# Kernel tuning notes

Measured on AMD Instinct MI355X. Metric: run time of the kernel, lower is better.

The kernel has to match this reference:

```python
import jax, jax.numpy as jnp
import numpy as np

B, T, C, H, W = 1, 8, 64, 96, 96
DG = 16  # deform groups
MAX_RES = 5.0  # max_residue_magnitude


def lrelu(x):
    return jnp.where(x >= 0, x, 0.1 * x)


def conv(x, w, b):
    y = jax.lax.conv_general_dilated(x, w, (1, 1), 'SAME',
                                     dimension_numbers=('NCHW', 'OIHW', 'NCHW'))
    return y + b[None, :, None, None]


def mod_deform_conv2d(x, offset, mask, weight, bias, dg):
    # Modulated deformable conv v2: 3x3 kernel, stride 1, pad 1, dil 1.
    Bs, Cin, Hs, Ws = x.shape
    K = 9
    cpg = Cin // dg
    Cout = weight.shape[0]
    off = offset.reshape(Bs, dg, K, 2, Hs, Ws)  # (y, x) per tap
    m = mask.reshape(Bs, dg, K, Hs, Ws)
    ky = jnp.repeat(jnp.arange(3), 3).astype(x.dtype)
    kx = jnp.tile(jnp.arange(3), 3).astype(x.dtype)
    # base sampling positions: out_pos - pad + tap*dil
    py = (jnp.arange(Hs, dtype=x.dtype) - 1.0)[None, :, None] + ky[:, None, None]  # (K,H,1)
    px = (jnp.arange(Ws, dtype=x.dtype) - 1.0)[None, None, :] + kx[:, None, None]  # (K,1,W)
    sy = off[:, :, :, 0] + py  # (B,dg,K,H,W)
    sx = off[:, :, :, 1] + px
    y0 = jnp.floor(sy)
    x0 = jnp.floor(sx)
    fy = sy - y0
    fx = sx - x0
    y0i = y0.astype(jnp.int32)
    x0i = x0.astype(jnp.int32)
    xf = x.reshape(Bs, dg, cpg, Hs * Ws)

    def gather(yi, xi, wgt):
        valid = (yi >= 0) & (yi < Hs) & (xi >= 0) & (xi < Ws)
        idx = (jnp.clip(yi, 0, Hs - 1) * Ws + jnp.clip(xi, 0, Ws - 1))
        idx = idx.reshape(Bs, dg, 1, K * Hs * Ws)
        v = jnp.take_along_axis(xf, idx, axis=3).reshape(Bs, dg, cpg, K, Hs, Ws)
        return v * (wgt * valid)[:, :, None]

    val = (gather(y0i, x0i, (1 - fy) * (1 - fx))
           + gather(y0i, x0i + 1, (1 - fy) * fx)
           + gather(y0i + 1, x0i, fy * (1 - fx))
           + gather(y0i + 1, x0i + 1, fy * fx))
    cols = val * m[:, :, None]  # (B,dg,cpg,K,H,W)
    wr = weight.reshape(Cout, dg, cpg, K)
    out = jnp.einsum('ogck,bgckhw->bohw', wr, cols)
    return out + bias[None, :, None, None]


def deform_align(xin, cond, p):
    h = lrelu(conv(cond, p['ow1'], p['ob1']))
    h = lrelu(conv(h, p['ow2'], p['ob2']))
    h = lrelu(conv(h, p['ow3'], p['ob3']))
    out = conv(h, p['ow4'], p['ob4'])
    offset = MAX_RES * jnp.tanh(out[:, :18 * DG])
    mask = jax.nn.sigmoid(out[:, 18 * DG:])
    return mod_deform_conv2d(xin, offset, mask, p['dw'], p['db'], DG)


def bidir_prop(x, params):
    t = x.shape[1]
    spatial = [x[:, i] for i in range(t)]
    feats = {}
    for name, rev in (('backward_', True), ('forward_', False)):
        p = params[name]
        order = list(range(t))[::-1] if rev else list(range(t))
        out_list = []
        prop = jnp.zeros_like(spatial[0])
        for i, idx in enumerate(order):
            cur = spatial[idx]
            if i > 0:
                feat_n2 = out_list[-2] if i > 1 else jnp.zeros_like(prop)
                cond = jnp.concatenate([prop, cur, feat_n2], axis=1)
                prop = deform_align(jnp.concatenate([prop, feat_n2], axis=1), cond, p)
            if name == 'forward_':
                feat = jnp.concatenate([cur, feats['backward_'][idx], prop], axis=1)
            else:
                feat = jnp.concatenate([cur, prop], axis=1)
            prop = prop + conv(lrelu(conv(feat, p['bw1'], p['bb1'])), p['bw2'], p['bb2'])
            out_list.append(prop)
        feats[name] = out_list[::-1] if rev else out_list
    fw, fb = params['fusion']
    outs = [conv(jnp.concatenate([feats['backward_'][i], feats['forward_'][i]], axis=1), fw, fb)
            for i in range(t)]
    return jnp.stack(outs, axis=1) + x


def setup_inputs() -> dict:
    key = jax.random.key(0)
    ks = iter(jax.random.split(key, 64))

    def w(*shape):
        return jax.random.normal(next(ks), shape, jnp.float32) * 0.03

    def b(n):
        return jnp.zeros((n,), jnp.float32)

    d = {'x': jax.random.normal(next(ks), (B, T, C, H, W), jnp.float32)}
    for pre, bb1_in in (('b', 2 * C), ('f', 3 * C)):
        d[pre + '_dw'] = w(C, 2 * C, 3, 3); d[pre + '_db'] = b(C)
        d[pre + '_ow1'] = w(C, 3 * C, 3, 3); d[pre + '_ob1'] = b(C)
        d[pre + '_ow2'] = w(C, C, 3, 3); d[pre + '_ob2'] = b(C)
        d[pre + '_ow3'] = w(C, C, 3, 3); d[pre + '_ob3'] = b(C)
        d[pre + '_ow4'] = w(27 * DG, C, 3, 3); d[pre + '_ob4'] = b(27 * DG)
        d[pre + '_bw1'] = w(C, bb1_in, 3, 3); d[pre + '_bb1'] = b(C)
        d[pre + '_bw2'] = w(C, C, 3, 3); d[pre + '_bb2'] = b(C)
    d['fus_w'] = w(C, 2 * C, 1, 1)
    d['fus_b'] = b(C)
    return d


def _assemble(b_dw, b_db, b_ow1, b_ob1, b_ow2, b_ob2, b_ow3, b_ob3, b_ow4, b_ob4,
              b_bw1, b_bb1, b_bw2, b_bb2,
              f_dw, f_db, f_ow1, f_ob1, f_ow2, f_ob2, f_ow3, f_ob3, f_ow4, f_ob4,
              f_bw1, f_bb1, f_bw2, f_bb2, fus_w, fus_b):
    return {
        'backward_': dict(dw=b_dw, db=b_db, ow1=b_ow1, ob1=b_ob1, ow2=b_ow2, ob2=b_ob2,
                          ow3=b_ow3, ob3=b_ob3, ow4=b_ow4, ob4=b_ob4,
                          bw1=b_bw1, bb1=b_bb1, bw2=b_bw2, bb2=b_bb2),
        'forward_': dict(dw=f_dw, db=f_db, ow1=f_ow1, ob1=f_ob1, ow2=f_ow2, ob2=f_ob2,
                         ow3=f_ow3, ob3=f_ob3, ow4=f_ow4, ob4=f_ob4,
                         bw1=f_bw1, bb1=f_bb1, bw2=f_bw2, bb2=f_bb2),
        'fusion': (fus_w, fus_b),
    }


def reference(x, b_dw, b_db, b_ow1, b_ob1, b_ow2, b_ob2, b_ow3, b_ob3, b_ow4, b_ob4,
              b_bw1, b_bb1, b_bw2, b_bb2,
              f_dw, f_db, f_ow1, f_ob1, f_ow2, f_ob2, f_ow3, f_ob3, f_ow4, f_ob4,
              f_bw1, f_bb1, f_bw2, f_bb2, fus_w, fus_b):
    params = _assemble(b_dw, b_db, b_ow1, b_ob1, b_ow2, b_ob2, b_ow3, b_ob3, b_ow4, b_ob4,
                       b_bw1, b_bb1, b_bw2, b_bb2,
                       f_dw, f_db, f_ow1, f_ob1, f_ow2, f_ob2, f_ow3, f_ob3, f_ow4, f_ob4,
                       f_bw1, f_bb1, f_bw2, f_bb2, fus_w, fus_b)
    return bidir_prop(x, params)
```

## Files before the change

### kernel.cpp

```cpp
#include <hip/hip_runtime.h>
#include <cstddef>
#include <cstdint>

#define HW96 9216
#define FRAME (64 * 9216)

typedef unsigned short ushort_t;
typedef __attribute__((ext_vector_type(8))) short bf16x8;
typedef __attribute__((ext_vector_type(4))) float f32x4;
typedef __attribute__((ext_vector_type(4))) unsigned u32x4;
typedef __attribute__((ext_vector_type(8))) ushort_t u16x8;
typedef __attribute__((ext_vector_type(4))) ushort_t u16x4;

__device__ __forceinline__ float unpk(unsigned p) {
    return __uint_as_float(p & 0xFFFF0000u) + __uint_as_float(p << 16);
}
__device__ __forceinline__ unsigned pk(float v) {
    unsigned u = __float_as_uint(v);
    unsigned hi = u & 0xFFFF0000u;
    float rem = v - __uint_as_float(hi);
    unsigned r = __float_as_uint(rem);
    unsigned lo = (r + 0x7FFFu + ((r >> 16) & 1u)) >> 16;
    return hi | (lo & 0xFFFFu);
}
__device__ __forceinline__ void split16(float v, ushort_t& h, ushort_t& l) {
    unsigned u = __float_as_uint(v);
    h = (ushort_t)(u >> 16);
    float rem = v - __uint_as_float(u & 0xFFFF0000u);
    unsigned r = __float_as_uint(rem);
    l = (ushort_t)((r + 0x7FFFu + ((r >> 16) & 1u)) >> 16);
}
__device__ __forceinline__ ushort_t bf16rnd(float v) {
    unsigned u = __float_as_uint(v);
    return (ushort_t)((u + 0x7FFFu + ((u >> 16) & 1u)) >> 16);
}
__device__ __forceinline__ float bfh(ushort_t h) {
    return __uint_as_float(((unsigned)h) << 16);
}

struct FragJob { const float* src; ushort_t* dst; int O, I, OT, KC, mode; };
struct FragJobs { FragJob j[15]; };

__global__ __launch_bounds__(256) void frag_all_k(FragJobs jobs) {
    const FragJob& J = jobs.j[blockIdx.y];
    int idx = blockIdx.x * 256 + threadIdx.x;
    int total = ((J.mode == 0) ? 9 : 1) * J.KC * J.OT * 512;
    if (idx >= total) return;
    int jj = idx & 7;
    int lane = (idx >> 3) & 63;
    int rem = idx >> 9;
    int ot = rem % J.OT;
    rem /= J.OT;
    int cc = rem % J.KC;
    int t = rem / J.KC;
    int o = ot * 16 + (lane & 15);
    float wv = 0.f;
    if (J.mode == 0) {
        int ci = cc * 32 + (lane >> 4) * 8 + jj;
        if (o < J.O && ci < J.I) wv = J.src[(o * J.I + ci) * 9 + t];
    } else if (J.mode == 1) {
        int K = cc * 32 + (lane >> 4) * 8 + jj;
        int g = K / 72, r2 = K % 72;
        int tap = r2 >> 3, c = r2 & 7;
        int ci = g * 8 + c;
        if (o < J.O && ci < J.I) wv = J.src[(o * J.I + ci) * 9 + tap];
    } else {
        int ci = cc * 32 + (lane >> 4) * 8 + jj;
        if (o < J.O && ci < J.I) wv = J.src[o * J.I + ci];
    }
    ushort_t h, l;
    split16(wv, h, l);
    J.dst[idx] = h;
    J.dst[total + idx] = l;
}

__global__ __launch_bounds__(256) void pack_tr_k(const float* __restrict__ src,
                                                 unsigned* __restrict__ dst,
                                                 ushort_t* __restrict__ dsth) {
    const int t = blockIdx.y;
    const int px0 = blockIdx.x * 64;
    __shared__ unsigned tile[64 * 65];
    const float* s = src + (size_t)t * FRAME;
    unsigned* d = dst + (size_t)t * FRAME;
    ushort_t* dh = dsth + (size_t)t * FRAME;
#pragma unroll
    for (int it = 0; it < 16; ++it) {
        int e = it * 256 + threadIdx.x;
        int p = e & 63, ch = e >> 6;
        tile[ch * 65 + p] = pk(s[(size_t)ch * HW96 + px0 + p]);
    }
    __syncthreads();
#pragma unroll
    for (int it = 0; it < 16; ++it) {
        int e = it * 256 + threadIdx.x;
        int ch = e & 63, p = e >> 6;
        unsigned v = tile[ch * 65 + p];
        d[(size_t)(px0 + p) * 64 + ch] = v;
        dh[(size_t)(px0 + p) * 64 + ch] = (ushort_t)(v >> 16);
    }
}

template <int TERMS>
__global__ __launch_bounds__(128, 3) void convm_k(
    const unsigned* __restrict__ s0, const unsigned* __restrict__ s1,
    int nsrc, int dslot, const float* __restrict__ dpacc,
    const float* __restrict__ ddbias, const ushort_t* __restrict__ wfrag,
    int KCfull, const float* __restrict__ bias,
    const float* __restrict__ addsrc, const float* __restrict__ addsrc2,
    const float* __restrict__ abias, ushort_t* __restrict__ outhi,
    unsigned* __restrict__ outpk, int act) {
    const int tid = threadIdx.x;
    const int lane = tid & 63;
    const int w = tid >> 6;
    const int h = blockIdx.x & 1;
    const int bseg = blockIdx.x >> 1;
    const int ot = h * 2 + w;
    const int xb = (bseg % 6) * 16;
    const int y = bseg / 6;
    const int n = lane & 15;
    const int quad = lane >> 4;

    __shared__ __align__(16) ushort_t ldsH[3 * 18 * 72];
    __shared__ __align__(16) ushort_t ldsL[3 * 18 * 72];

    int jst[4], jok[4], joff[4], jbase[4];
#pragma unroll
    for (int i = 0; i < 4; ++i) {
        int e = tid + i * 128;
        int rc = e >> 3, cg = e & 7;
        int r = rc / 18, col = rc - r * 18;
        int gy = y - 1 + r, gx = xb - 1 + col;
        jst[i] = (e < 432);
        jok[i] = jst[i] && ((unsigned)gy < 96u) && ((unsigned)gx < 96u);
        joff[i] = (gy * 96 + gx) * 64 + cg * 8;
        jbase[i] = rc * 72 + cg * 8;
    }

    f32x4 acc0, acc1;
#pragma unroll
    for (int r = 0; r < 4; ++r) { acc0[r] = 0.f; acc1[r] = 0.f; }

    const size_t hlOff = (size_t)9 * KCfull * 4 * 512;

    for (int j = 0; j < nsrc; ++j) {
        const int base = j * 2;
        __syncthreads();
        if (j == dslot) {
#pragma unroll
            for (int i = 0; i < 4; ++i) {
                if (jst[i]) {
                    ushort_t hh[8], ll[8];
                    if (jok[i]) {
                        const int cg8 = ((tid + i * 128) & 7) << 3;
                        f32x4 a0 = *(const f32x4*)(dpacc + joff[i]);
                        f32x4 a1 = *(const f32x4*)(dpacc + joff[i] + 4);
                        f32x4 b0 = *(const f32x4*)(dpacc + FRAME + joff[i]);
                        f32x4 b1 = *(const f32x4*)(dpacc + FRAME + joff[i] + 4);
                        f32x4 d0 = *(const f32x4*)(ddbias + cg8);
                        f32x4 d1 = *(const f32x4*)(ddbias + cg8 + 4);
#pragma unroll
                        for (int q = 0; q < 4; ++q) {
                            split16(a0[q] + b0[q] + d0[q], hh[q], ll[q]);
                            split16(a1[q] + b1[q] + d1[q], hh[4 + q], ll[4 + q]);
                        }
                    } else {
#pragma unroll
                        for (int q = 0; q < 8; ++q) { hh[q] = 0; ll[q] = 0; }
                    }
                    u32x4 H, L;
#pragma unroll
                    for (int q = 0; q < 4; ++q) {
                        H[q] = (unsigned)hh[2 * q] | ((unsigned)hh[2 * q + 1] << 16);
                        L[q] = (unsigned)ll[2 * q] | ((unsigned)ll[2 * q + 1] << 16);
                    }
                    *(u32x4*)(ldsH + jbase[i]) = H;
                    *(u32x4*)(ldsL + jbase[i]) = L;
                }
            }
        } else {
            const unsigned* sv = (j == 0) ? s0 : s1;
#pragma unroll
            for (int i = 0; i < 4; ++i) {
                if (jst[i]) {
                    u32x4 a, b;
                    if (jok[i]) {
                        a = *(const u32x4*)(sv + joff[i]);
                        b = *(const u32x4*)(sv + joff[i] + 4);
                    } else {
#pragma unroll
                        for (int q = 0; q < 4; ++q) { a[q] = 0; b[q] = 0; }
                    }
                    u32x4 H, L;
#pragma unroll
                    for (int q = 0; q < 2; ++q) {
                        H[q] = (a[2 * q] >> 16) | (a[2 * q + 1] & 0xFFFF0000u);
                        L[q] = (a[2 * q] & 0xFFFFu) | (a[2 * q + 1] << 16);
                        H[2 + q] = (b[2 * q] >> 16) | (b[2 * q + 1] & 0xFFFF0000u);
                        L[2 + q] = (b[2 * q] & 0xFFFFu) | (b[2 * q + 1] << 16);
                    }
                    *(u32x4*)(ldsH + jbase[i]) = H;
                    *(u32x4*)(ldsL + jbase[i]) = L;
                }
            }
        }
        __syncthreads();
        bf16x8 pAh[5], pAl[5], pBh[5], pBl[5];
#pragma unroll
        for (int s = 0; s < 23; ++s) {
            if (s >= 5) {
                const int u = s - 5;
                const bf16x8 Ah = pAh[u % 5];
                const bf16x8 Bh = pBh[u % 5], Bl = pBl[u % 5];
                if (u & 1) {
                    acc1 = __builtin_amdgcn_mfma_f32_16x16x32_bf16(Ah, Bh, acc1, 0, 0, 0);
                    if (TERMS == 3)
                        acc1 = __builtin_amdgcn_mfma_f32_16x16x32_bf16(pAl[u % 5], Bh, acc1, 0, 0, 0);
                    acc1 = __builtin_amdgcn_mfma_f32_16x16x32_bf16(Ah, Bl, acc1, 0, 0, 0);
                } else {
                    acc0 = __builtin_amdgcn_mfma_f32_16x16x32_bf16(Ah, Bh, acc0, 0, 0, 0);
                    if (TERMS == 3)
                        acc0 = __builtin_amdgcn_mfma_f32_16x16x32_bf16(pAl[u % 5], Bh, acc0, 0, 0, 0);
                    acc0 = __builtin_amdgcn_mfma_f32_16x16x32_bf16(Ah, Bl, acc0, 0, 0, 0);
                }
            }
            if (s < 18) {
                const int t = s >> 1, cc2 = s & 1;
                const int ky = t / 3, kx = t % 3;
                const int ccor = base + cc2;
                const ushort_t* ab =
                    wfrag + (((size_t)(t * KCfull + ccor) * 4 + ot) * 64 + lane) * 8;
                pAh[s % 5] = *(const bf16x8*)ab;
                if (TERMS == 3) pAl[s % 5] = *(const bf16x8*)(ab + hlOff);
                const int lb = (ky * 18 + n + kx) * 72 + cc2 * 32 + quad * 8;
                pBh[s % 5] = *(const bf16x8*)(ldsH + lb);
                pBl[s % 5] = *(const bf16x8*)(ldsL + lb);
            }
        }
    }

    const int px = y * 96 + xb + n;
    f32x4 pa, pb;
#pragma unroll
    for (int r = 0; r < 4; ++r) { pa[r] = 0.f; pb[r] = 0.f; }
    if (addsrc) {
        pa = *(const f32x4*)(addsrc + (size_t)px * 64 + ot * 16 + quad * 4);
        pb = *(const f32x4*)(addsrc2 + (size_t)px * 64 + ot * 16 + quad * 4);
    }
    u16x4 hi4;
#pragma unroll
    for (int r = 0; r < 4; ++r) {
        int cout = ot * 16 + quad * 4 + r;
        float v = acc0[r] + acc1[r] + bias[cout];
        if (act) v = (v >= 0.f) ? v : 0.1f * v;
        if (addsrc) v += pa[r] + pb[r] + abias[cout];
        outpk[(size_t)px * 64 + cout] = pk(v);
        hi4[r] = bf16rnd(v);
    }
    if (outhi)
        *(u16x4*)(outhi + (size_t)px * 64 + ot * 16 + quad * 4) = hi4;
}

__global__ __launch_bounds__(128, 3) void convh_k(
    const ushort_t* __restrict__ s0, const ushort_t* __restrict__ s1,
    const ushort_t* __restrict__ s2, int b0, int b1, int b2, int nsrc,
    const ushort_t* __restrict__ wfrag, int KCfull,
    const float* __restrict__ bias, ushort_t* __restrict__ outhi, int act) {
    const int tid = threadIdx.x;
    const int lane = tid & 63;
    const int w = tid >> 6;
    const int h = blockIdx.x & 1;
    const int bseg = blockIdx.x >> 1;
    const int ot = h * 2 + w;
    const int xb = (bseg % 6) * 16;
    const int y = bseg / 6;
    const int n = lane & 15;
    const int quad = lane >> 4;

    __shared__ __align__(16) ushort_t ldsH[3 * 18 * 72];

    int jst[4], jok[4], joff[4], jbase[4];
#pragma unroll
    for (int i = 0; i < 4; ++i) {
        int e = tid + i * 128;
        int rc = e >> 3, cg = e & 7;
        int r = rc / 18, col = rc - r * 18;
        int gy = y - 1 + r, gx = xb - 1 + col;
        jst[i] = (e < 432);
        jok[i] = jst[i] && ((unsigned)gy < 96u) && ((unsigned)gx < 96u);
        joff[i] = (gy * 96 + gx) * 64 + cg * 8;
        jbase[i] = rc * 72 + cg * 8;
    }

    f32x4 acc0, acc1;
#pragma unroll
    for (int r = 0; r < 4; ++r) { acc0[r] = 0.f; acc1[r] = 0.f; }

    for (int j = 0; j < nsrc; ++j) {
        const ushort_t* sv = (j == 0) ? s0 : (j == 1 ? s1 : s2);
        const int base = (j == 0) ? b0 : (j == 1 ? b1 : b2);
        __syncthreads();
#pragma unroll
        for (int i = 0; i < 4; ++i) {
            if (jst[i]) {
                u16x8 a;
                if (jok[i]) {
                    a = *(const u16x8*)(sv + joff[i]);
                } else {
#pragma unroll
                    for (int q = 0; q < 8; ++q) a[q] = 0;
                }
                *(u16x8*)(ldsH + jbase[i]) = a;
            }
        }
        __syncthreads();
        bf16x8 pAh[5], pBh[5];
#pragma unroll
        for (int s = 0; s < 23; ++s) {
            if (s >= 5) {
                const int u = s - 5;
                const bf16x8 Ah = pAh[u % 5];
                const bf16x8 Bh = pBh[u % 5];
                if (u & 1)
                    acc1 = __builtin_amdgcn_mfma_f32_16x16x32_bf16(Ah, Bh, acc1, 0, 0, 0);
                else
                    acc0 = __builtin_amdgcn_mfma_f32_16x16x32_bf16(Ah, Bh, acc0, 0, 0, 0);
            }
            if (s < 18) {
                const int t = s >> 1, cc2 = s & 1;
                const int ky = t / 3, kx = t % 3;
                const int ccor = base + cc2;
                const ushort_t* ab =
                    wfrag + (((size_t)(t * KCfull + ccor) * 4 + ot) * 64 + lane) * 8;
                pAh[s % 5] = *(const bf16x8*)ab;
                const int lb = (ky * 18 + n + kx) * 72 + cc2 * 32 + quad * 8;
                pBh[s % 5] = *(const bf16x8*)(ldsH + lb);
            }
        }
    }

    const int px = y * 96 + xb + n;
    u16x4 hi4;
#pragma unroll
    for (int r = 0; r < 4; ++r) {
        int cout = ot * 16 + quad * 4 + r;
        float v = acc0[r] + acc1[r] + bias[cout];
        if (act) v = (v >= 0.f) ? v : 0.1f * v;
        hi4[r] = bf16rnd(v);
    }
    *(u16x4*)(outhi + (size_t)px * 64 + ot * 16 + quad * 4) = hi4;
}

__global__ __launch_bounds__(256) void dconv_fused_k(
    const ushort_t* __restrict__ sAh, const ushort_t* __restrict__ sBh,
    const ushort_t* __restrict__ hAh, const ushort_t* __restrict__ w4,
    const float* __restrict__ ob4, const ushort_t* __restrict__ dwf,
    int ngr4, float* __restrict__ pacc) {
    const int tid = threadIdx.x;
    const int lane = tid & 63;
    const int w = tid >> 6;
    const int h = blockIdx.x & 1;
    const int seg = blockIdx.x >> 1;
    const int xb = (seg % 6) * 16;
    const int y = seg / 6;
    const int n = lane & 15;
    const int quad = lane >> 4;

    __shared__ __align__(16) char smem[15232 + 9472];
    float* rawS = (float*)smem;
    ushort_t* ldsAH = (ushort_t*)(smem + 15232);
    ushort_t* colsH = (ushort_t*)(smem + 15232);

    const int nrounds = ngr4 >> 1;
    const int ng = nrounds * 4;
    const int g0 = h * ng;
    const int otO_s = (g0 * 18) >> 4;
    const int otO_e = (g0 * 18 + ng * 18 - 1) >> 4;
    const int nO = otO_e - otO_s + 1;
    const int otM_s = (288 + g0 * 9) >> 4;
    const int otM_e = (288 + g0 * 9 + ng * 9 - 1) >> 4;
    const int nM = otM_e - otM_s + 1;
    const int nt = nO + nM;
    const int rowOffO = otO_s * 16;
    const int rowOffM = otM_s * 16 - nO * 16;

#pragma unroll
    for (int i = 0; i < 2; ++i) {
        int e = tid + i * 256;
        if (e < 432) {
            int rc = e >> 3, cg = e & 7;
            int r = rc / 18, col = rc - r * 18;
            int gy = y - 1 + r, gx = xb - 1 + col;
            bool ok = ((unsigned)gy < 96u) && ((unsigned)gx < 96u);
            u16x8 a;
            if (ok) {
                a = *(const u16x8*)(hAh + (gy * 96 + gx) * 64 + cg * 8);
            } else {
#pragma unroll
                for (int q = 0; q < 8; ++q) a[q] = 0;
            }
            *(u16x8*)(ldsAH + rc * 72 + cg * 8) = a;
        }
    }
    __syncthreads();

#pragma unroll 1
    for (int j = 0; j < 4; ++j) {
        const int idx = j * 4 + w;
        if (idx >= nt) break;
        const int ot = (idx < nO) ? (otO_s + idx) : (otM_s + (idx - nO));
        f32x4 a0, a1;
#pragma unroll
        for (int r = 0; r < 4; ++r) { a0[r] = 0.f; a1[r] = 0.f; }
        bf16x8 pAh[5], pBh[5];
#pragma unroll
        for (int s = 0; s < 23; ++s) {
            if (s >= 5) {
                const int u = s - 5;
                const bf16x8 Ah = pAh[u % 5];
                const bf16x8 Bh = pBh[u % 5];
                if (u & 1)
                    a1 = __builtin_amdgcn_mfma_f32_16x16x32_bf16(Ah, Bh, a1, 0, 0, 0);
                else
                    a0 = __builtin_amdgcn_mfma_f32_16x16x32_bf16(Ah, Bh, a0, 0, 0, 0);
            }
            if (s < 18) {
                const int t = s >> 1, cc2 = s & 1;
                const int ky = t / 3, kx = t % 3;
                const ushort_t* ab =
                    w4 + (((size_t)s * 28 + ot) * 64 + lane) * 8;
                pAh[s % 5] = *(const bf16x8*)ab;
                const int lb = (ky * 18 + n + kx) * 72 + cc2 * 32 + quad * 8;
                pBh[s % 5] = *(const bf16x8*)(ldsAH + lb);
            }
        }
#pragma unroll
        for (int r = 0; r < 4; ++r) {
            int cout = ot * 16 + quad * 4 + r;
            float v = a0[r] + a1[r] + (cout < 432 ? ob4[cout] : 0.f);
            rawS[(idx * 16 + quad * 4 + r) * 17 + n] = v;
        }
    }

    f32x4 acc0, acc1;
#pragma unroll
    for (int r = 0; r < 4; ++r) { acc0[r] = 0.f; acc1[r] = 0.f; }

    for (int gci = 0; gci < nrounds; ++gci) {
        const int gc = h * nrounds + gci;
        __syncthreads();
#pragma unroll
        for (int i = 0; i < 3; ++i) {
            int e = tid + i * 256;
            if (e < 576) {
                int p = e & 15;
                int r = e >> 4;
                int gl = r / 9, k = r - gl * 9;
                int g = gc * 4 + gl;
                float ry = rawS[(g * 18 + k * 2 + 0 - rowOffO) * 17 + p];
                float rx = rawS[(g * 18 + k * 2 + 1 - rowOffO) * 17 + p];
                float rm = rawS[(288 + g * 9 + k - rowOffM) * 17 + p];
                float oy = 5.f * (1.f - 2.f / (1.f + __expf(2.f * ry)));
                float ox = 5.f * (1.f - 2.f / (1.f + __expf(2.f * rx)));
                float m = 1.f / (1.f + __expf(-rm));
                float sy = oy + (float)(y - 1 + k / 3);
                float sx = ox + (float)(xb + p - 1 + k % 3);
                float fy0 = floorf(sy), fx0 = floorf(sx);
                float fy = sy - fy0, fx = sx - fx0;
                int y0 = (int)fy0, x0 = (int)fx0;
                int y1 = y0 + 1, x1 = x0 + 1;
                bool vy0 = (unsigned)y0 < 96u, vy1 = (unsigned)y1 < 96u;
                bool vx0 = (unsigned)x0 < 96u, vx1 = (unsigned)x1 < 96u;
                int cy0 = min(max(y0, 0), 95), cy1 = min(max(y1, 0), 95);
                int cx0 = min(max(x0, 0), 95), cx1 = min(max(x1, 0), 95);
                float w00 = (1.f - fy) * (1.f - fx) * ((vy0 && vx0) ? 1.f : 0.f);
                float w01 = (1.f - fy) * fx * ((vy0 && vx1) ? 1.f : 0.f);
                float w10 = fy * (1.f - fx) * ((vy1 && vx0) ? 1.f : 0.f);
                float w11 = fy * fx * ((vy1 && vx1) ? 1.f : 0.f);
                const ushort_t* src = (g < 8) ? sAh : sBh;
                int cb = (g & 7) * 8;
                int kbase = p * 296 + gl * 72 + k * 8;
                ushort_t hh[8];
                if (src) {
                    u16x8 c00 = *(const u16x8*)(src + (cy0 * 96 + cx0) * 64 + cb);
                    u16x8 c01 = *(const u16x8*)(src + (cy0 * 96 + cx1) * 64 + cb);
                    u16x8 c10 = *(const u16x8*)(src + (cy1 * 96 + cx0) * 64 + cb);
                    u16x8 c11 = *(const u16x8*)(src + (cy1 * 96 + cx1) * 64 + cb);
#pragma unroll
                    for (int c = 0; c < 8; ++c) {
                        float v = w00 * bfh(c00[c]) + w01 * bfh(c01[c]) +
                                  w10 * bfh(c10[c]) + w11 * bfh(c11[c]);
                        hh[c] = bf16rnd(v * m);
                    }
                } else {
#pragma unroll
                    for (int c = 0; c < 8; ++c) hh[c] = 0;
                }
                u32x4 H;
#pragma unroll
                for (int q = 0; q < 4; ++q)
                    H[q] = (unsigned)hh[2 * q] | ((unsigned)hh[2 * q + 1] << 16);
                *(u32x4*)(colsH + kbase) = H;
            }
        }
        __syncthreads();
        bf16x8 qAh[4], qBh[4];
#pragma unroll
        for (int s = 0; s < 13; ++s) {
            if (s >= 4) {
                const int u = s - 4;
                const bf16x8 Ah = qAh[u % 4];
                const bf16x8 Bh = qBh[u % 4];
                if (u & 1)
                    acc1 = __builtin_amdgcn_mfma_f32_16x16x32_bf16(Ah, Bh, acc1, 0, 0, 0);
                else
                    acc0 = __builtin_amdgcn_mfma_f32_16x16x32_bf16(Ah, Bh, acc0, 0, 0, 0);
            }
            if (s < 9) {
                const int cc = gc * 9 + s;
                const ushort_t* ab = dwf + (((size_t)cc * 4 + w) * 64 + lane) * 8;
                qAh[s % 4] = *(const bf16x8*)ab;
                const int lb = n * 296 + s * 32 + quad * 8;
                qBh[s % 4] = *(const bf16x8*)(colsH + lb);
            }
        }
    }

    const int pidx = y * 96 + xb + n;
    f32x4 sv;
#pragma unroll
    for (int r = 0; r < 4; ++r) sv[r] = acc0[r] + acc1[r];
    *(f32x4*)(pacc + (size_t)h * FRAME + (size_t)pidx * 64 + w * 16 +
              quad * 4) = sv;
}

__global__ __launch_bounds__(128) void fusem_k(
    const unsigned* __restrict__ featB, const unsigned* __restrict__ featF,
    const float* __restrict__ x, const ushort_t* __restrict__ wfrag,
    const float* __restrict__ bias, float* __restrict__ out) {
    const int tid = threadIdx.x;
    const int lane = tid & 63;
    const int w = tid >> 6;
    const int h = blockIdx.x & 1;
    const int bseg = blockIdx.x >> 1;
    const int t = blockIdx.y;
    const int ot = h * 2 + w;
    const int xb = (bseg % 6) * 16;
    const int y = bseg / 6;
    const int n = lane & 15;
    const int quad = lane >> 4;

    __shared__ __align__(16) ushort_t ldsH[16 * 144];
    __shared__ __align__(16) ushort_t ldsL[16 * 144];

    const int p = tid >> 3, cg = tid & 7;
    const int off = ((y * 96 + xb + p) * 64 + cg * 8);
#pragma unroll
    for (int i = 0; i < 2; ++i) {
        const unsigned* sv =
            (i == 0 ? featB : featF) + (size_t)t * FRAME;
        u32x4 a = *(const u32x4*)(sv + off);
        u32x4 b = *(const u32x4*)(sv + off + 4);
        u32x4 H, L;
#pragma unroll
        for (int q = 0; q < 2; ++q) {
            H[q] = (a[2 * q] >> 16) | (a[2 * q + 1] & 0xFFFF0000u);
            L[q] = (a[2 * q] & 0xFFFFu) | (a[2 * q + 1] << 16);
            H[2 + q] = (b[2 * q] >> 16) | (b[2 * q + 1] & 0xFFFF0000u);
            L[2 + q] = (b[2 * q] & 0xFFFFu) | (b[2 * q + 1] << 16);
        }
        *(u32x4*)(ldsH + p * 144 + i * 64 + cg * 8) = H;
        *(u32x4*)(ldsL + p * 144 + i * 64 + cg * 8) = L;
    }
    __syncthreads();

    f32x4 acc0, acc1;
#pragma unroll
    for (int r = 0; r < 4; ++r) { acc0[r] = 0.f; acc1[r] = 0.f; }
    const size_t hlOff = (size_t)4 * 4 * 512;
#pragma unroll
    for (int cc = 0; cc < 4; ++cc) {
        const ushort_t* ab = wfrag + (((size_t)cc * 4 + ot) * 64 + lane) * 8;
        bf16x8 Ah = *(const bf16x8*)ab;
        bf16x8 Al = *(const bf16x8*)(ab + hlOff);
        int lb = n * 144 + cc * 32 + quad * 8;
        bf16x8 Bh = *(const bf16x8*)(ldsH + lb);
        bf16x8 Bl = *(const bf16x8*)(ldsL + lb);
        if (cc & 1) {
            acc1 = __builtin_amdgcn_mfma_f32_16x16x32_bf16(Ah, Bh, acc1, 0, 0, 0);
            acc1 = __builtin_amdgcn_mfma_f32_16x16x32_bf16(Al, Bh, acc1, 0, 0, 0);
            acc1 = __builtin_amdgcn_mfma_f32_16x16x32_bf16(Ah, Bl, acc1, 0, 0, 0);
        } else {
            acc0 = __builtin_amdgcn_mfma_f32_16x16x32_bf16(Ah, Bh, acc0, 0, 0, 0);
            acc0 = __builtin_amdgcn_mfma_f32_16x16x32_bf16(Al, Bh, acc0, 0, 0, 0);
            acc0 = __builtin_amdgcn_mfma_f32_16x16x32_bf16(Ah, Bl, acc0, 0, 0, 0);
        }
    }

    const int pidx = y * 96 + xb + n;
    const float* xt = x + (size_t)t * FRAME;
    float* od = out + (size_t)t * FRAME;
#pragma unroll
    for (int r = 0; r < 4; ++r) {
        int cout = ot * 16 + quad * 4 + r;
        size_t o2 = (size_t)cout * HW96 + pidx;
        od[o2] = acc0[r] + acc1[r] + bias[cout] + xt[o2];
    }
}

extern "C" void kernel_launch(void* const* d_in, const int* in_sizes, int n_in,
                              void* d_out, int out_size, void* d_ws,
                              size_t ws_size, hipStream_t stream) {
    const float* x = (const float*)d_in[0];
    auto gp = [&](int i) { return (const float*)d_in[i]; };

    struct DirP {
        const float *dw, *db, *ow1, *ob1, *ow2, *ob2, *ow3, *ob3, *ow4, *ob4,
            *bw1, *bb1, *bw2, *bb2;
    };
    DirP Pb{gp(1), gp(2), gp(3), gp(4), gp(5), gp(6), gp(7),
            gp(8), gp(9), gp(10), gp(11), gp(12), gp(13), gp(14)};
    DirP Pf{gp(15), gp(16), gp(17), gp(18), gp(19), gp(20), gp(21),
            gp(22), gp(23), gp(24), gp(25), gp(26), gp(27), gp(28)};
    const float* fus_w = gp(29);
    const float* fus_b = gp(30);

    unsigned* featBpk = (unsigned*)d_ws;
    unsigned* featFpk = featBpk + (size_t)8 * FRAME;
    unsigned* xpk = featFpk + (size_t)8 * FRAME;
    unsigned* hApk = xpk + (size_t)8 * FRAME;
    unsigned* hBpk = hApk + FRAME;
    ushort_t* fragp = (ushort_t*)(hBpk + FRAME);

    auto falloc = [&](size_t nelem) {
        ushort_t* p = fragp;
        fragp += nelem;
        return p;
    };

    struct DirW { ushort_t *ow1, *ow2, *ow3, *ow4, *bw1, *bw2, *dw; int bw1KC; };
    FragJobs fj;
    int nf = 0;
    auto fjob = [&](const float* src, int O, int I, int OT, int KC) {
        ushort_t* dst = falloc((size_t)2 * 9 * KC * OT * 512);
        fj.j[nf++] = FragJob{src, dst, O, I, OT, KC, 0};
        return dst;
    };
    auto fjobd = [&](const float* src) {
        ushort_t* dst = falloc((size_t)2 * 36 * 4 * 512);
        fj.j[nf++] = FragJob{src, dst, 64, 128, 4, 36, 1};
        return dst;
    };
    DirW Wb, Wf;
    Wb.ow1 = fjob(Pb.ow1, 64, 192, 4, 6);
    Wb.ow2 = fjob(Pb.ow2, 64, 64, 4, 2);
    Wb.ow3 = fjob(Pb.ow3, 64, 64, 4, 2);
    Wb.ow4 = fjob(Pb.ow4, 432, 64, 28, 2);
    Wb.bw1 = fjob(Pb.bw1, 64, 128, 4, 4);
    Wb.bw1KC = 4;
    Wb.bw2 = fjob(Pb.bw2, 64, 64, 4, 2);
    Wb.dw = fjobd(Pb.dw);
    Wf.ow1 = fjob(Pf.ow1, 64, 192, 4, 6);
    Wf.ow2 = fjob(Pf.ow2, 64, 64, 4, 2);
    Wf.ow3 = fjob(Pf.ow3, 64, 64, 4, 2);
    Wf.ow4 = fjob(Pf.ow4, 432, 64, 28, 2);
    Wf.bw1 = fjob(Pf.bw1, 64, 192, 4, 6);
    Wf.bw1KC = 6;
    Wf.bw2 = fjob(Pf.bw2, 64, 64, 4, 2);
    Wf.dw = fjobd(Pf.dw);
    ushort_t* Wfus = falloc((size_t)2 * 4 * 4 * 512);
    fj.j[nf++] = FragJob{fus_w, Wfus, 64, 128, 4, 4, 2};
    frag_all_k<<<dim3(1008, 15), 256, 0, stream>>>(fj);

    float* pacc = (float*)((((uintptr_t)fragp) + 15) & ~(uintptr_t)15);
    ushort_t* featBh = (ushort_t*)(pacc + (size_t)2 * FRAME);
    ushort_t* featFh = featBh + (size_t)8 * FRAME;
    ushort_t* xh = featFh + (size_t)8 * FRAME;
    ushort_t* hAh = (ushort_t*)hApk;
    ushort_t* hBh = (ushort_t*)hBpk;

    pack_tr_k<<<dim3(144, 8), 256, 0, stream>>>(x, xpk, xh);

    auto convm = [&](const unsigned* a, const unsigned* b, int withD,
                     const float* ddbias, const ushort_t* frag, int KCfull,
                     const float* bias, const float* add, const float* add2,
                     const float* abias, ushort_t* outhi, unsigned* out,
                     int act, int terms) {
        const unsigned* S[2] = {nullptr, nullptr};
        int ns = 0;
        if (a) S[ns++] = a;
        if (b) S[ns++] = b;
        int dslot = -1;
        if (withD) { dslot = ns; ++ns; }
        if (terms == 2)
            convm_k<2><<<1152, 128, 0, stream>>>(
                S[0], S[1], ns, dslot, pacc, ddbias, frag, KCfull, bias, add,
                add2, abias, outhi, out, act);
        else
            convm_k<3><<<1152, 128, 0, stream>>>(
                S[0], S[1], ns, dslot, pacc, ddbias, frag, KCfull, bias, add,
                add2, abias, outhi, out, act);
    };

    auto convh = [&](const ushort_t* a, const ushort_t* b, const ushort_t* c2,
                     const ushort_t* frag, int KCfull, const float* bias,
                     ushort_t* out, int act) {
        const ushort_t* srcs[3] = {a, b, c2};
        const ushort_t* S[3] = {nullptr, nullptr, nullptr};
        int B[3] = {0, 0, 0};
        int ns = 0;
        for (int j = 0; j < 3; ++j)
            if (srcs[j]) {
                S[ns] = srcs[j];
                B[ns] = j * 2;
                ++ns;
            }
        convh_k<<<1152, 128, 0, stream>>>(S[0], S[1], S[2], B[0], B[1], B[2],
                                          ns, frag, KCfull, bias, out, act);
    };

    for (int dir = 0; dir < 2; ++dir) {
        const DirP& P = dir ? Pf : Pb;
        const DirW& W = dir ? Wf : Wb;
        unsigned* feat = dir ? featFpk : featBpk;
        ushort_t* feath = dir ? featFh : featBh;
        const ushort_t* prev1h = nullptr;
        const ushort_t* prev2h = nullptr;
        for (int i = 0; i < 8; ++i) {
            int idx = dir ? i : 7 - i;
            const unsigned* cur = xpk + (size_t)idx * FRAME;
            const ushort_t* curh = xh + (size_t)idx * FRAME;
            bool hasD = false;
            if (i > 0) {
                convh(prev1h, curh, prev2h, W.ow1, 6, P.ob1, hAh, 1);
                convh(hAh, nullptr, nullptr, W.ow2, 2, P.ob2, hBh, 1);
                convh(hBh, nullptr, nullptr, W.ow3, 2, P.ob3, hAh, 1);
                int ngr4 = (prev2h != nullptr) ? 4 : 2;
                dconv_fused_k<<<1152, 256, 0, stream>>>(
                    prev1h, prev2h, hAh, W.ow4, P.ob4, W.dw, ngr4, pacc);
                hasD = true;
            }
            unsigned* dst = feat + (size_t)idx * FRAME;
            ushort_t* dsth = feath + (size_t)idx * FRAME;
            if (dir == 0) {
                convm(cur, nullptr, hasD ? 1 : 0, P.db, W.bw1, W.bw1KC, P.bb1,
                      nullptr, nullptr, nullptr, nullptr, hBpk, 1, 2);
            } else {
                convm(cur, featBpk + (size_t)idx * FRAME, hasD ? 1 : 0, P.db,
                      W.bw1, W.bw1KC, P.bb1, nullptr, nullptr, nullptr,
                      nullptr, hBpk, 1, 2);
            }
            convm(hBpk, nullptr, 0, nullptr, W.bw2, 2, P.bb2,
                  hasD ? pacc : nullptr, pacc + FRAME, P.db, dsth, dst, 0, 2);
            prev2h = prev1h;
            prev1h = dsth;
        }
    }

    fusem_k<<<dim3(1152, 8), 128, 0, stream>>>(featBpk, featFpk, x, Wfus,
                                               fus_b, (float*)d_out);
}
```

Before: 1.153 ms.

## Drop split-bf16 hi/lo precision in backbone convs and fusion, use plain bf16

Replaces the packed hi+lo (split bf16) activation storage and the 2-term MFMA backbone convolution with a single-bf16 convolution kernel, and removes the low-part activation term in the fusion kernel. Activations, features and the input frames are now stored only as bf16, which halves activation memory traffic and LDS use and cuts MFMA count in the backbone and fusion. The cost is reduced numerical accuracy, since activations lose their residual low-order bits, which may push results toward the tolerance limit.

```diff
diff --git a/kernel.cpp b/kernel.cpp
--- a/kernel.cpp
+++ b/kernel.cpp
@@ -12,17 +12,6 @@
 typedef __attribute__((ext_vector_type(8))) ushort_t u16x8;
 typedef __attribute__((ext_vector_type(4))) ushort_t u16x4;
 
-__device__ __forceinline__ float unpk(unsigned p) {
-    return __uint_as_float(p & 0xFFFF0000u) + __uint_as_float(p << 16);
-}
-__device__ __forceinline__ unsigned pk(float v) {
-    unsigned u = __float_as_uint(v);
-    unsigned hi = u & 0xFFFF0000u;
-    float rem = v - __uint_as_float(hi);
-    unsigned r = __float_as_uint(rem);
-    unsigned lo = (r + 0x7FFFu + ((r >> 16) & 1u)) >> 16;
-    return hi | (lo & 0xFFFFu);
-}
 __device__ __forceinline__ void split16(float v, ushort_t& h, ushort_t& l) {
     unsigned u = __float_as_uint(v);
     h = (ushort_t)(u >> 16);
@@ -75,189 +64,25 @@
 }
 
 __global__ __launch_bounds__(256) void pack_tr_k(const float* __restrict__ src,
-                                                 unsigned* __restrict__ dst,
                                                  ushort_t* __restrict__ dsth) {
     const int t = blockIdx.y;
     const int px0 = blockIdx.x * 64;
-    __shared__ unsigned tile[64 * 65];
+    __shared__ ushort_t tile[64 * 65];
     const float* s = src + (size_t)t * FRAME;
-    unsigned* d = dst + (size_t)t * FRAME;
     ushort_t* dh = dsth + (size_t)t * FRAME;
 #pragma unroll
     for (int it = 0; it < 16; ++it) {
         int e = it * 256 + threadIdx.x;
         int p = e & 63, ch = e >> 6;
-        tile[ch * 65 + p] = pk(s[(size_t)ch * HW96 + px0 + p]);
+        tile[ch * 65 + p] = bf16rnd(s[(size_t)ch * HW96 + px0 + p]);
     }
     __syncthreads();
 #pragma unroll
     for (int it = 0; it < 16; ++it) {
         int e = it * 256 + threadIdx.x;
         int ch = e & 63, p = e >> 6;
-        unsigned v = tile[ch * 65 + p];
-        d[(size_t)(px0 + p) * 64 + ch] = v;
-        dh[(size_t)(px0 + p) * 64 + ch] = (ushort_t)(v >> 16);
-    }
-}
-
-template <int TERMS>
-__global__ __launch_bounds__(128, 3) void convm_k(
-    const unsigned* __restrict__ s0, const unsigned* __restrict__ s1,
-    int nsrc, int dslot, const float* __restrict__ dpacc,
-    const float* __restrict__ ddbias, const ushort_t* __restrict__ wfrag,
-    int KCfull, const float* __restrict__ bias,
-    const float* __restrict__ addsrc, const float* __restrict__ addsrc2,
-    const float* __restrict__ abias, ushort_t* __restrict__ outhi,
-    unsigned* __restrict__ outpk, int act) {
-    const int tid = threadIdx.x;
-    const int lane = tid & 63;
-    const int w = tid >> 6;
-    const int h = blockIdx.x & 1;
-    const int bseg = blockIdx.x >> 1;
-    const int ot = h * 2 + w;
-    const int xb = (bseg % 6) * 16;
-    const int y = bseg / 6;
-    const int n = lane & 15;
-    const int quad = lane >> 4;
-
-    __shared__ __align__(16) ushort_t ldsH[3 * 18 * 72];
-    __shared__ __align__(16) ushort_t ldsL[3 * 18 * 72];
-
-    int jst[4], jok[4], joff[4], jbase[4];
-#pragma unroll
-    for (int i = 0; i < 4; ++i) {
-        int e = tid + i * 128;
-        int rc = e >> 3, cg = e & 7;
-        int r = rc / 18, col = rc - r * 18;
-        int gy = y - 1 + r, gx = xb - 1 + col;
-        jst[i] = (e < 432);
-        jok[i] = jst[i] && ((unsigned)gy < 96u) && ((unsigned)gx < 96u);
-        joff[i] = (gy * 96 + gx) * 64 + cg * 8;
-        jbase[i] = rc * 72 + cg * 8;
-    }
-
-    f32x4 acc0, acc1;
-#pragma unroll
-    for (int r = 0; r < 4; ++r) { acc0[r] = 0.f; acc1[r] = 0.f; }
-
-    const size_t hlOff = (size_t)9 * KCfull * 4 * 512;
-
-    for (int j = 0; j < nsrc; ++j) {
-        const int base = j * 2;
-        __syncthreads();
-        if (j == dslot) {
-#pragma unroll
-            for (int i = 0; i < 4; ++i) {
-                if (jst[i]) {
-                    ushort_t hh[8], ll[8];
-                    if (jok[i]) {
-                        const int cg8 = ((tid + i * 128) & 7) << 3;
-                        f32x4 a0 = *(const f32x4*)(dpacc + joff[i]);
-                        f32x4 a1 = *(const f32x4*)(dpacc + joff[i] + 4);
-                        f32x4 b0 = *(const f32x4*)(dpacc + FRAME + joff[i]);
-                        f32x4 b1 = *(const f32x4*)(dpacc + FRAME + joff[i] + 4);
-                        f32x4 d0 = *(const f32x4*)(ddbias + cg8);
-                        f32x4 d1 = *(const f32x4*)(ddbias + cg8 + 4);
-#pragma unroll
-                        for (int q = 0; q < 4; ++q) {
-                            split16(a0[q] + b0[q] + d0[q], hh[q], ll[q]);
-                            split16(a1[q] + b1[q] + d1[q], hh[4 + q], ll[4 + q]);
-                        }
-                    } else {
-#pragma unroll
-                        for (int q = 0; q < 8; ++q) { hh[q] = 0; ll[q] = 0; }
-                    }
-                    u32x4 H, L;
-#pragma unroll
-                    for (int q = 0; q < 4; ++q) {
-                        H[q] = (unsigned)hh[2 * q] | ((unsigned)hh[2 * q + 1] << 16);
-                        L[q] = (unsigned)ll[2 * q] | ((unsigned)ll[2 * q + 1] << 16);
-                    }
-                    *(u32x4*)(ldsH + jbase[i]) = H;
-                    *(u32x4*)(ldsL + jbase[i]) = L;
-                }
-            }
-        } else {
-            const unsigned* sv = (j == 0) ? s0 : s1;
-#pragma unroll
-            for (int i = 0; i < 4; ++i) {
-                if (jst[i]) {
-                    u32x4 a, b;
-                    if (jok[i]) {
-                        a = *(const u32x4*)(sv + joff[i]);
-                        b = *(const u32x4*)(sv + joff[i] + 4);
-                    } else {
-#pragma unroll
-                        for (int q = 0; q < 4; ++q) { a[q] = 0; b[q] = 0; }
-                    }
-                    u32x4 H, L;
-#pragma unroll
-                    for (int q = 0; q < 2; ++q) {
-                        H[q] = (a[2 * q] >> 16) | (a[2 * q + 1] & 0xFFFF0000u);
-                        L[q] = (a[2 * q] & 0xFFFFu) | (a[2 * q + 1] << 16);
-                        H[2 + q] = (b[2 * q] >> 16) | (b[2 * q + 1] & 0xFFFF0000u);
-                        L[2 + q] = (b[2 * q] & 0xFFFFu) | (b[2 * q + 1] << 16);
-                    }
-                    *(u32x4*)(ldsH + jbase[i]) = H;
-                    *(u32x4*)(ldsL + jbase[i]) = L;
-                }
-            }
-        }
-        __syncthreads();
-        bf16x8 pAh[5], pAl[5], pBh[5], pBl[5];
-#pragma unroll
-        for (int s = 0; s < 23; ++s) {
-            if (s >= 5) {
-                const int u = s - 5;
-                const bf16x8 Ah = pAh[u % 5];
-                const bf16x8 Bh = pBh[u % 5], Bl = pBl[u % 5];
-                if (u & 1) {
-                    acc1 = __builtin_amdgcn_mfma_f32_16x16x32_bf16(Ah, Bh, acc1, 0, 0, 0);
-                    if (TERMS == 3)
-                        acc1 = __builtin_amdgcn_mfma_f32_16x16x32_bf16(pAl[u % 5], Bh, acc1, 0, 0, 0);
-                    acc1 = __builtin_amdgcn_mfma_f32_16x16x32_bf16(Ah, Bl, acc1, 0, 0, 0);
-                } else {
-                    acc0 = __builtin_amdgcn_mfma_f32_16x16x32_bf16(Ah, Bh, acc0, 0, 0, 0);
-                    if (TERMS == 3)
-                        acc0 = __builtin_amdgcn_mfma_f32_16x16x32_bf16(pAl[u % 5], Bh, acc0, 0, 0, 0);
-                    acc0 = __builtin_amdgcn_mfma_f32_16x16x32_bf16(Ah, Bl, acc0, 0, 0, 0);
-                }
-            }
-            if (s < 18) {
-                const int t = s >> 1, cc2 = s & 1;
-                const int ky = t / 3, kx = t % 3;
-                const int ccor = base + cc2;
-                const ushort_t* ab =
-                    wfrag + (((size_t)(t * KCfull + ccor) * 4 + ot) * 64 + lane) * 8;
-                pAh[s % 5] = *(const bf16x8*)ab;
-                if (TERMS == 3) pAl[s % 5] = *(const bf16x8*)(ab + hlOff);
-                const int lb = (ky * 18 + n + kx) * 72 + cc2 * 32 + quad * 8;
-                pBh[s % 5] = *(const bf16x8*)(ldsH + lb);
-                pBl[s % 5] = *(const bf16x8*)(ldsL + lb);
-            }
-        }
-    }
-
-    const int px = y * 96 + xb + n;
-    f32x4 pa, pb;
-#pragma unroll
-    for (int r = 0; r < 4; ++r) { pa[r] = 0.f; pb[r] = 0.f; }
-    if (addsrc) {
-        pa = *(const f32x4*)(addsrc + (size_t)px * 64 + ot * 16 + quad * 4);
-        pb = *(const f32x4*)(addsrc2 + (size_t)px * 64 + ot * 16 + quad * 4);
-    }
-    u16x4 hi4;
-#pragma unroll
-    for (int r = 0; r < 4; ++r) {
-        int cout = ot * 16 + quad * 4 + r;
-        float v = acc0[r] + acc1[r] + bias[cout];
-        if (act) v = (v >= 0.f) ? v : 0.1f * v;
-        if (addsrc) v += pa[r] + pb[r] + abias[cout];
-        outpk[(size_t)px * 64 + cout] = pk(v);
-        hi4[r] = bf16rnd(v);
-    }
-    if (outhi)
-        *(u16x4*)(outhi + (size_t)px * 64 + ot * 16 + quad * 4) = hi4;
+        dh[(size_t)(px0 + p) * 64 + ch] = tile[ch * 65 + p];
+    }
 }
 
 __global__ __launch_bounds__(128, 3) void convh_k(
@@ -345,6 +170,135 @@
         int cout = ot * 16 + quad * 4 + r;
         float v = acc0[r] + acc1[r] + bias[cout];
         if (act) v = (v >= 0.f) ? v : 0.1f * v;
+        hi4[r] = bf16rnd(v);
+    }
+    *(u16x4*)(outhi + (size_t)px * 64 + ot * 16 + quad * 4) = hi4;
+}
+
+__global__ __launch_bounds__(128, 3) void convb_k(
+    const ushort_t* __restrict__ s0, const ushort_t* __restrict__ s1,
+    int nsrc, int dslot, const float* __restrict__ dpacc,
+    const float* __restrict__ ddbias, const ushort_t* __restrict__ wfrag,
+    int KCfull, const float* __restrict__ bias,
+    const float* __restrict__ addsrc, const float* __restrict__ addsrc2,
+    const float* __restrict__ abias, ushort_t* __restrict__ outhi, int act) {
+    const int tid = threadIdx.x;
+    const int lane = tid & 63;
+    const int w = tid >> 6;
+    const int h = blockIdx.x & 1;
+    const int bseg = blockIdx.x >> 1;
+    const int ot = h * 2 + w;
+    const int xb = (bseg % 6) * 16;
+    const int y = bseg / 6;
+    const int n = lane & 15;
+    const int quad = lane >> 4;
+
+    __shared__ __align__(16) ushort_t ldsH[3 * 18 * 72];
+
+    int jst[4], jok[4], joff[4], jbase[4];
+#pragma unroll
+    for (int i = 0; i < 4; ++i) {
+        int e = tid + i * 128;
+        int rc = e >> 3, cg = e & 7;
+        int r = rc / 18, col = rc - r * 18;
+        int gy = y - 1 + r, gx = xb - 1 + col;
+        jst[i] = (e < 432);
+        jok[i] = jst[i] && ((unsigned)gy < 96u) && ((unsigned)gx < 96u);
+        joff[i] = (gy * 96 + gx) * 64 + cg * 8;
+        jbase[i] = rc * 72 + cg * 8;
+    }
+
+    f32x4 acc0, acc1;
+#pragma unroll
+    for (int r = 0; r < 4; ++r) { acc0[r] = 0.f; acc1[r] = 0.f; }
+
+    for (int j = 0; j < nsrc; ++j) {
+        const int base = j * 2;
+        __syncthreads();
+        if (j == dslot) {
+#pragma unroll
+            for (int i = 0; i < 4; ++i) {
+                if (jst[i]) {
+                    u16x8 a;
+                    if (jok[i]) {
+                        const int cg8 = ((tid + i * 128) & 7) << 3;
+                        f32x4 a0 = *(const f32x4*)(dpacc + joff[i]);
+                        f32x4 a1 = *(const f32x4*)(dpacc + joff[i] + 4);
+                        f32x4 b0 = *(const f32x4*)(dpacc + FRAME + joff[i]);
+                        f32x4 b1 = *(const f32x4*)(dpacc + FRAME + joff[i] + 4);
+                        f32x4 d0 = *(const f32x4*)(ddbias + cg8);
+                        f32x4 d1 = *(const f32x4*)(ddbias + cg8 + 4);
+#pragma unroll
+                        for (int q = 0; q < 4; ++q) {
+                            a[q] = bf16rnd(a0[q] + b0[q] + d0[q]);
+                            a[4 + q] = bf16rnd(a1[q] + b1[q] + d1[q]);
+                        }
+                    } else {
+#pragma unroll
+                        for (int q = 0; q < 8; ++q) a[q] = 0;
+                    }
+                    *(u16x8*)(ldsH + jbase[i]) = a;
+                }
+            }
+        } else {
+            const ushort_t* sv = (j == 0) ? s0 : s1;
+#pragma unroll
+            for (int i = 0; i < 4; ++i) {
+                if (jst[i]) {
+                    u16x8 a;
+                    if (jok[i]) {
+                        a = *(const u16x8*)(sv + joff[i]);
+                    } else {
+#pragma unroll
+                        for (int q = 0; q < 8; ++q) a[q] = 0;
+                    }
+                    *(u16x8*)(ldsH + jbase[i]) = a;
+                }
+            }
+        }
+        __syncthreads();
+        bf16x8 pAh[5], pBh[5];
+#pragma unroll
+        for (int s = 0; s < 23; ++s) {
+            if (s >= 5) {
+                const int u = s - 5;
+                const bf16x8 Ah = pAh[u % 5];
+                const bf16x8 Bh = pBh[u % 5];
+                if (u & 1)
+                    acc1 = __builtin_amdgcn_mfma_f32_16x16x32_bf16(Ah, Bh, acc1, 0, 0, 0);
+                else
+                    acc0 = __builtin_amdgcn_mfma_f32_16x16x32_bf16(Ah, Bh, acc0, 0, 0, 0);
+            }
+            if (s < 18) {
+                const int t = s >> 1, cc2 = s & 1;
+                const int ky = t / 3, kx = t % 3;
+                const int ccor = j * 2 + cc2;
+                (void)ccor;
+                const int cco = base + cc2;
+                const ushort_t* ab =
+                    wfrag + (((size_t)(t * KCfull + cco) * 4 + ot) * 64 + lane) * 8;
+                pAh[s % 5] = *(const bf16x8*)ab;
+                const int lb = (ky * 18 + n + kx) * 72 + cc2 * 32 + quad * 8;
+                pBh[s % 5] = *(const bf16x8*)(ldsH + lb);
+            }
+        }
+    }
+
+    const int px = y * 96 + xb + n;
+    f32x4 pa, pb;
+#pragma unroll
+    for (int r = 0; r < 4; ++r) { pa[r] = 0.f; pb[r] = 0.f; }
+    if (addsrc) {
+        pa = *(const f32x4*)(addsrc + (size_t)px * 64 + ot * 16 + quad * 4);
+        pb = *(const f32x4*)(addsrc2 + (size_t)px * 64 + ot * 16 + quad * 4);
+    }
+    u16x4 hi4;
+#pragma unroll
+    for (int r = 0; r < 4; ++r) {
+        int cout = ot * 16 + quad * 4 + r;
+        float v = acc0[r] + acc1[r] + bias[cout];
+        if (act) v = (v >= 0.f) ? v : 0.1f * v;
+        if (addsrc) v += pa[r] + pb[r] + abias[cout];
         hi4[r] = bf16rnd(v);
     }
     *(u16x4*)(outhi + (size_t)px * 64 + ot * 16 + quad * 4) = hi4;
@@ -534,7 +488,7 @@
 }
 
 __global__ __launch_bounds__(128) void fusem_k(
-    const unsigned* __restrict__ featB, const unsigned* __restrict__ featF,
+    const ushort_t* __restrict__ featBh, const ushort_t* __restrict__ featFh,
     const float* __restrict__ x, const ushort_t* __restrict__ wfrag,
     const float* __restrict__ bias, float* __restrict__ out) {
     const int tid = threadIdx.x;
@@ -550,26 +504,15 @@
     const int quad = lane >> 4;
 
     __shared__ __align__(16) ushort_t ldsH[16 * 144];
-    __shared__ __align__(16) ushort_t ldsL[16 * 144];
 
     const int p = tid >> 3, cg = tid & 7;
     const int off = ((y * 96 + xb + p) * 64 + cg * 8);
 #pragma unroll
     for (int i = 0; i < 2; ++i) {
-        const unsigned* sv =
-            (i == 0 ? featB : featF) + (size_t)t * FRAME;
-        u32x4 a = *(const u32x4*)(sv + off);
-        u32x4 b = *(const u32x4*)(sv + off + 4);
-        u32x4 H, L;
-#pragma unroll
-        for (int q = 0; q < 2; ++q) {
-            H[q] = (a[2 * q] >> 16) | (a[2 * q + 1] & 0xFFFF0000u);
-            L[q] = (a[2 * q] & 0xFFFFu) | (a[2 * q + 1] << 16);
-            H[2 + q] = (b[2 * q] >> 16) | (b[2 * q + 1] & 0xFFFF0000u);
-            L[2 + q] = (b[2 * q] & 0xFFFFu) | (b[2 * q + 1] << 16);
-        }
-        *(u32x4*)(ldsH + p * 144 + i * 64 + cg * 8) = H;
-        *(u32x4*)(ldsL + p * 144 + i * 64 + cg * 8) = L;
+        const ushort_t* sv =
+            (i == 0 ? featBh : featFh) + (size_t)t * FRAME;
+        u16x8 a = *(const u16x8*)(sv + off);
+        *(u16x8*)(ldsH + p * 144 + i * 64 + cg * 8) = a;
     }
     __syncthreads();
 
@@ -584,15 +527,12 @@
         bf16x8 Al = *(const bf16x8*)(ab + hlOff);
         int lb = n * 144 + cc * 32 + quad * 8;
         bf16x8 Bh = *(const bf16x8*)(ldsH + lb);
-        bf16x8 Bl = *(const bf16x8*)(ldsL + lb);
         if (cc & 1) {
             acc1 = __builtin_amdgcn_mfma_f32_16x16x32_bf16(Ah, Bh, acc1, 0, 0, 0);
             acc1 = __builtin_amdgcn_mfma_f32_16x16x32_bf16(Al, Bh, acc1, 0, 0, 0);
-            acc1 = __builtin_amdgcn_mfma_f32_16x16x32_bf16(Ah, Bl, acc1, 0, 0, 0);
         } else {
             acc0 = __builtin_amdgcn_mfma_f32_16x16x32_bf16(Ah, Bh, acc0, 0, 0, 0);
             acc0 = __builtin_amdgcn_mfma_f32_16x16x32_bf16(Al, Bh, acc0, 0, 0, 0);
-            acc0 = __builtin_amdgcn_mfma_f32_16x16x32_bf16(Ah, Bl, acc0, 0, 0, 0);
         }
     }
 
@@ -624,12 +564,13 @@
     const float* fus_w = gp(29);
     const float* fus_b = gp(30);
 
-    unsigned* featBpk = (unsigned*)d_ws;
-    unsigned* featFpk = featBpk + (size_t)8 * FRAME;
-    unsigned* xpk = featFpk + (size_t)8 * FRAME;
-    unsigned* hApk = xpk + (size_t)8 * FRAME;
-    unsigned* hBpk = hApk + FRAME;
-    ushort_t* fragp = (ushort_t*)(hBpk + FRAME);
+    ushort_t* xh = (ushort_t*)d_ws;
+    ushort_t* featBh = xh + (size_t)8 * FRAME;
+    ushort_t* featFh = featBh + (size_t)8 * FRAME;
+    ushort_t* hAh = featFh + (size_t)8 * FRAME;
+    ushort_t* hBh = hAh + FRAME;
+    float* pacc = (float*)((((uintptr_t)(hBh + FRAME)) + 15) & ~(uintptr_t)15);
+    ushort_t* fragp = (ushort_t*)(pacc + (size_t)2 * FRAME);
 
     auto falloc = [&](size_t nelem) {
         ushort_t* p = fragp;
@@ -671,35 +612,7 @@
     fj.j[nf++] = FragJob{fus_w, Wfus, 64, 128, 4, 4, 2};
     frag_all_k<<<dim3(1008, 15), 256, 0, stream>>>(fj);
 
-    float* pacc = (float*)((((uintptr_t)fragp) + 15) & ~(uintptr_t)15);
-    ushort_t* featBh = (ushort_t*)(pacc + (size_t)2 * FRAME);
-    ushort_t* featFh = featBh + (size_t)8 * FRAME;
-    ushort_t* xh = featFh + (size_t)8 * FRAME;
-    ushort_t* hAh = (ushort_t*)hApk;
-    ushort_t* hBh = (ushort_t*)hBpk;
-
-    pack_tr_k<<<dim3(144, 8), 256, 0, stream>>>(x, xpk, xh);
-
-    auto convm = [&](const unsigned* a, const unsigned* b, int withD,
-                     const float* ddbias, const ushort_t* frag, int KCfull,
-                     const float* bias, const float* add, const float* add2,
-                     const float* abias, ushort_t* outhi, unsigned* out,
-                     int act, int terms) {
-        const unsigned* S[2] = {nullptr, nullptr};
-        int ns = 0;
-        if (a) S[ns++] = a;
-        if (b) S[ns++] = b;
-        int dslot = -1;
-        if (withD) { dslot = ns; ++ns; }
-        if (terms == 2)
-            convm_k<2><<<1152, 128, 0, stream>>>(
-                S[0], S[1], ns, dslot, pacc, ddbias, frag, KCfull, bias, add,
-                add2, abias, outhi, out, act);
-        else
-            convm_k<3><<<1152, 128, 0, stream>>>(
-                S[0], S[1], ns, dslot, pacc, ddbias, frag, KCfull, bias, add,
-                add2, abias, outhi, out, act);
-    };
+    pack_tr_k<<<dim3(144, 8), 256, 0, stream>>>(x, xh);
 
     auto convh = [&](const ushort_t* a, const ushort_t* b, const ushort_t* c2,
                      const ushort_t* frag, int KCfull, const float* bias,
@@ -718,16 +631,29 @@
                                           ns, frag, KCfull, bias, out, act);
     };
 
+    auto convb = [&](const ushort_t* a, const ushort_t* b, int withD,
+                     const float* ddbias, const ushort_t* frag, int KCfull,
+                     const float* bias, const float* add, const float* add2,
+                     const float* abias, ushort_t* out, int act) {
+        const ushort_t* S[2] = {nullptr, nullptr};
+        int ns = 0;
+        if (a) S[ns++] = a;
+        if (b) S[ns++] = b;
+        int dslot = -1;
+        if (withD) { dslot = ns; ++ns; }
+        convb_k<<<1152, 128, 0, stream>>>(S[0], S[1], ns, dslot, pacc, ddbias,
+                                          frag, KCfull, bias, add, add2,
+                                          abias, out, act);
+    };
+
     for (int dir = 0; dir < 2; ++dir) {
         const DirP& P = dir ? Pf : Pb;
         const DirW& W = dir ? Wf : Wb;
-        unsigned* feat = dir ? featFpk : featBpk;
         ushort_t* feath = dir ? featFh : featBh;
         const ushort_t* prev1h = nullptr;
         const ushort_t* prev2h = nullptr;
         for (int i = 0; i < 8; ++i) {
             int idx = dir ? i : 7 - i;
-            const unsigned* cur = xpk + (size_t)idx * FRAME;
             const ushort_t* curh = xh + (size_t)idx * FRAME;
             bool hasD = false;
             if (i > 0) {
@@ -739,23 +665,22 @@
                     prev1h, prev2h, hAh, W.ow4, P.ob4, W.dw, ngr4, pacc);
                 hasD = true;
             }
-            unsigned* dst = feat + (size_t)idx * FRAME;
             ushort_t* dsth = feath + (size_t)idx * FRAME;
             if (dir == 0) {
-                convm(cur, nullptr, hasD ? 1 : 0, P.db, W.bw1, W.bw1KC, P.bb1,
-                      nullptr, nullptr, nullptr, nullptr, hBpk, 1, 2);
+                convb(curh, nullptr, hasD ? 1 : 0, P.db, W.bw1, W.bw1KC,
+                      P.bb1, nullptr, nullptr, nullptr, hBh, 1);
             } else {
-                convm(cur, featBpk + (size_t)idx * FRAME, hasD ? 1 : 0, P.db,
-                      W.bw1, W.bw1KC, P.bb1, nullptr, nullptr, nullptr,
-                      nullptr, hBpk, 1, 2);
-            }
-            convm(hBpk, nullptr, 0, nullptr, W.bw2, 2, P.bb2,
-                  hasD ? pacc : nullptr, pacc + FRAME, P.db, dsth, dst, 0, 2);
+                convb(curh, featBh + (size_t)idx * FRAME, hasD ? 1 : 0, P.db,
+                      W.bw1, W.bw1KC, P.bb1, nullptr, nullptr, nullptr, hBh,
+                      1);
+            }
+            convb(hBh, nullptr, 0, nullptr, W.bw2, 2, P.bb2,
+                  hasD ? pacc : nullptr, pacc + FRAME, P.db, dsth, 0);
             prev2h = prev1h;
             prev1h = dsth;
         }
     }
 
-    fusem_k<<<dim3(1152, 8), 128, 0, stream>>>(featBpk, featFpk, x, Wfus,
+    fusem_k<<<dim3(1152, 8), 128, 0, stream>>>(featBh, featFh, x, Wfus,
                                                fus_b, (float*)d_out);
 }
```

New measurement: 1.063 ms. 7.8% less time.
